# Performance work log

Measured on AMD Instinct MI355X. Metric: run time of the kernel, lower is better.

Reference implementation:

```python
import jax, jax.numpy as jnp
import numpy as np

EPS = 1e-08
SLOPE = 0.01  # LeakyReLU default negative_slope
B = 2097152
H = 32

def leaky_relu(x):
    return jnp.where(x >= 0, x, SLOPE * x)

def gram_schmidt(v, w):
    # v, w: [b,3]
    v_on = v / (jnp.linalg.norm(v, axis=-1, keepdims=True) + EPS)
    proj = jnp.sum(w * v_on, axis=-1, keepdims=True) * v_on
    w_orth = w - proj
    w_on = w_orth / (jnp.linalg.norm(w_orth, axis=-1, keepdims=True) + EPS)
    u_on = jnp.cross(v_on, w_on)
    R = jnp.stack((v_on, w_on, u_on), axis=-1)  # [b,3,3]
    v_local = jnp.einsum('bji,bj->bi', R, v)    # R^T @ v
    w_local = jnp.einsum('bji,bj->bi', R, w)
    return R, v_local, w_local

def setup_inputs() -> dict:
    key = jax.random.key(0)
    ks = jax.random.split(key, 12)
    std = 0.0001  # init_weights() normal std
    return {
        'v': jax.random.normal(ks[0], (B, 3), jnp.float32),
        'w': jax.random.normal(ks[1], (B, 3), jnp.float32),
        'W1': jax.random.normal(ks[2], (H, 3), jnp.float32) * std,
        'b1': jax.random.normal(ks[3], (H,), jnp.float32) * std,
        'W2': jax.random.normal(ks[4], (H, H), jnp.float32) * std,
        'b2': jax.random.normal(ks[5], (H,), jnp.float32) * std,
        'Wd1': jax.random.normal(ks[6], (H, H), jnp.float32) * std,
        'bd1': jax.random.normal(ks[7], (H,), jnp.float32) * std,
        'Wd2': jax.random.normal(ks[8], (3, H), jnp.float32) * std,
        'bd2': jax.random.normal(ks[9], (3,), jnp.float32) * std,
        'bias': jnp.array([[0.0, 0.0, -9.81]], jnp.float32),
    }

def reference(v, w, W1, b1, W2, b2, Wd1, bd1, Wd2, bd2, bias):
    shapes = v.shape
    b = shapes[0]
    v = v.reshape(b, 3)
    w = w.reshape(b, 3)
    R, v_local, w_local = gram_schmidt(v, w)
    feat = jnp.concatenate([v_local[..., :1], w_local[..., :2]], axis=-1)  # [b,3]
    h1 = leaky_relu(feat @ W1.T + b1)           # [b,H]
    h = leaky_relu(h1 @ W2.T + b2) * h1         # [b,H]
    y = leaky_relu(h @ Wd1.T + bd1) @ Wd2.T + bd2  # [b,3]
    y = jnp.einsum('bij,bj->bi', R, y) + bias
    return y.reshape(shapes)
```

## Files before the change

kernel.cpp:

```cpp
#include <hip/hip_runtime.h>

typedef __attribute__((ext_vector_type(8))) short short8;
typedef __attribute__((ext_vector_type(4))) float f32x4;
typedef __attribute__((ext_vector_type(2))) float f32x2;
typedef __attribute__((ext_vector_type(4))) unsigned int u32x4;

static __device__ __forceinline__ unsigned int fbits(float f) {
    union { float f; unsigned int u; } v; v.f = f; return v.u;
}
static __device__ __forceinline__ float bitsf(unsigned int u) {
    union { float f; unsigned int u; } v; v.u = u; return v.f;
}
static __device__ __forceinline__ unsigned int pkbf(float lo, float hi) {
    return __builtin_amdgcn_perm(fbits(hi), fbits(lo), 0x07060302u);
}
static __device__ __forceinline__ float leaky(float x) { return fmaxf(x, 0.01f * x); }
static __device__ __forceinline__ float rsqrt_nr(float x) {
    const float r = __builtin_amdgcn_rsqf(x);
    return r * (1.5f - (0.5f * x) * (r * r));
}
static __device__ __forceinline__ f32x2 pk_mul_v(f32x2 a, f32x2 b) {
    f32x2 d; asm("v_pk_mul_f32 %0, %1, %2" : "=v"(d) : "v"(a), "v"(b)); return d;
}
static __device__ __forceinline__ f32x2 pk_fma_v(f32x2 a, f32x2 b, f32x2 c) {
    f32x2 d; asm("v_pk_fma_f32 %0, %1, %2, %3" : "=v"(d) : "v"(a), "v"(b), "v"(c)); return d;
}


struct Rot { float a0,a1,a2,c0,c1,c2,u0,u1,u2; };

static __device__ __forceinline__ Rot gs_feat(
    const float* __restrict__ vin, const float* __restrict__ win,
    int row, unsigned int* __restrict__ dst)
{
    const float v0 = vin[3*row+0], v1 = vin[3*row+1], v2 = vin[3*row+2];
    const float w0 = win[3*row+0], w1 = win[3*row+1], w2 = win[3*row+2];
    const float sv  = v0*v0 + v1*v1 + v2*v2;
    const float rnv = rsqrt_nr(sv);
    const float a0 = v0*rnv, a1 = v1*rnv, a2 = v2*rnv;
    const float proj = w0*a0 + w1*a1 + w2*a2;
    const float o0 = w0 - proj*a0, o1 = w1 - proj*a1, o2 = w2 - proj*a2;
    const float sw  = o0*o0 + o1*o1 + o2*o2;
    const float rnw = rsqrt_nr(sw);
    const float c0 = o0*rnw, c1 = o1*rnw, c2 = o2*rnw;
    const float u0 = a1*c2 - a2*c1;
    const float u1 = a2*c0 - a0*c2;
    const float u2 = a0*c1 - a1*c0;
    *(u32x4*)(dst)     = (u32x4){ fbits(sv*rnv) >> 16, fbits(proj) >> 16,
                                  fbits(sw*rnw) >> 16, 0u };
    *(u32x4*)(dst + 4) = (u32x4){ 0u, 0u, 0u, 0u };
    return {a0,a1,a2,c0,c1,c2,u0,u1,u2};
}

#define TILE_CHAIN(LB, YS0, YS1, YS2)                                              \
    {                                                                              \
        float y0k = 0.f, y1k = 0.f, y2k = 0.f;                                     \
        _Pragma("unroll")                                                          \
        for (int t = 0; t < 4; ++t) {                                              \
            const u32x4 bfr = *(const u32x4*)(                                     \
                &featlds[((LB) + wbase + 16*t + i15) * 8 + ko]);                   \
            const short8 featfrag = __builtin_bit_cast(short8, bfr);               \
            const f32x4 z1lo = __builtin_amdgcn_mfma_f32_16x16x32_bf16(            \
                fW1lo, featfrag, cb1lo, 0, 0, 0);                                  \
            const f32x4 z1hi = __builtin_amdgcn_mfma_f32_16x16x32_bf16(            \
                fW1hi, featfrag, cb1hi, 0, 0, 0);                                  \
            const float h1l0 = leaky(z1lo[0]), h1l1 = leaky(z1lo[1]);              \
            const float h1l2 = leaky(z1lo[2]), h1l3 = leaky(z1lo[3]);              \
            const float h1h0 = leaky(z1hi[0]), h1h1 = leaky(z1hi[1]);              \
            const float h1h2 = leaky(z1hi[2]), h1h3 = leaky(z1hi[3]);              \
            const short8 h1frag = __builtin_bit_cast(short8, (u32x4){              \
                pkbf(h1l0, h1h0), pkbf(h1l1, h1h1),                                \
                pkbf(h1l2, h1h2), pkbf(h1l3, h1h3) });                             \
            const f32x4 z2lo = __builtin_amdgcn_mfma_f32_16x16x32_bf16(            \
                fW2lo, h1frag, cb2lo, 0, 0, 0);                                    \
            const f32x4 z2hi = __builtin_amdgcn_mfma_f32_16x16x32_bf16(            \
                fW2hi, h1frag, cb2hi, 0, 0, 0);                                    \
            const short8 h2frag = __builtin_bit_cast(short8, (u32x4){              \
                pkbf(leaky(z2lo[0]) * h1l0, leaky(z2hi[0]) * h1h0),                \
                pkbf(leaky(z2lo[1]) * h1l1, leaky(z2hi[1]) * h1h1),                \
                pkbf(leaky(z2lo[2]) * h1l2, leaky(z2hi[2]) * h1h2),                \
                pkbf(leaky(z2lo[3]) * h1l3, leaky(z2hi[3]) * h1h3) });             \
            const f32x4 z3lo = __builtin_amdgcn_mfma_f32_16x16x32_bf16(            \
                fWd1lo, h2frag, cbd1lo, 0, 0, 0);                                  \
            const f32x4 z3hi = __builtin_amdgcn_mfma_f32_16x16x32_bf16(            \
                fWd1hi, h2frag, cbd1hi, 0, 0, 0);                                  \
            f32x2 h30, h31, h32, h33;                                              \
            h30.x = leaky(z3lo[0]); h30.y = leaky(z3hi[0]);                        \
            h31.x = leaky(z3lo[1]); h31.y = leaky(z3hi[1]);                        \
            h32.x = leaky(z3lo[2]); h32.y = leaky(z3hi[2]);                        \
            h33.x = leaky(z3lo[3]); h33.y = leaky(z3hi[3]);                        \
            f32x2 P0 = pk_mul_v(w00, h30);                                         \
            f32x2 P1 = pk_mul_v(w10, h30);                                         \
            f32x2 P2 = pk_mul_v(w20, h30);                                         \
            P0 = pk_fma_v(w01, h31, P0); P1 = pk_fma_v(w11, h31, P1);              \
            P2 = pk_fma_v(w21, h31, P2);                                           \
            P0 = pk_fma_v(w02, h32, P0); P1 = pk_fma_v(w12, h32, P1);              \
            P2 = pk_fma_v(w22, h32, P2);                                           \
            P0 = pk_fma_v(w03, h33, P0); P1 = pk_fma_v(w13, h33, P1);              \
            P2 = pk_fma_v(w23, h33, P2);                                           \
            float s0 = P0.x + P0.y, s1 = P1.x + P1.y, s2 = P2.x + P2.y;            \
            s0 += __shfl_xor(s0, 16); s0 += __shfl_xor(s0, 32);                    \
            s1 += __shfl_xor(s1, 16); s1 += __shfl_xor(s1, 32);                    \
            s2 += __shfl_xor(s2, 16); s2 += __shfl_xor(s2, 32);                    \
            if (quad == t) { y0k = s0; y1k = s1; y2k = s2; }                       \
        }                                                                          \
        YS0 = y0k; YS1 = y1k; YS2 = y2k;                                           \
    }

__global__ __launch_bounds__(256, 3) void aero_mfma(
    const float* __restrict__ vin, const float* __restrict__ win,
    const float* __restrict__ gW1, const float* __restrict__ gb1,
    const float* __restrict__ gW2, const float* __restrict__ gb2,
    const float* __restrict__ gWd1, const float* __restrict__ gbd1,
    const float* __restrict__ gWd2, const float* __restrict__ gbd2,
    const float* __restrict__ gbias,
    float* __restrict__ out, int nrows)
{
    __shared__ unsigned int featlds[513 * 8];

    const int tid   = threadIdx.x;
    const int i15   = tid & 15;
    const int quad  = (tid >> 4) & 3;
    const int wbase = tid & 192;
    const int ko    = 4 * quad;

    const int base = blockIdx.x * 512;
    int rowA = base + tid;        if (rowA >= nrows) rowA = nrows - 1;
    int rowB = base + 256 + tid;  if (rowB >= nrows) rowB = nrows - 1;

    unsigned int a1lo[4] = {0,0,0,0}, a1hi[4] = {0,0,0,0};
    if (quad == 0) {
        #pragma unroll
        for (int j = 0; j < 3; ++j) {
            a1lo[j] = fbits(gW1[i15 * 3 + j]) >> 16;
            a1hi[j] = fbits(gW1[(16 + i15) * 3 + j]) >> 16;
        }
    }
    const short8 fW1lo = __builtin_bit_cast(short8, (u32x4){a1lo[0], a1lo[1], a1lo[2], a1lo[3]});
    const short8 fW1hi = __builtin_bit_cast(short8, (u32x4){a1hi[0], a1hi[1], a1hi[2], a1hi[3]});

    unsigned int a2lo[4], a2hi[4], a3lo[4], a3hi[4];
    {
        const float* p;
        p = gW2 + i15 * 32 + ko;
        { f32x4 xa = *(const f32x4*)p, xb = *(const f32x4*)(p + 16);
          #pragma unroll
          for (int j = 0; j < 4; ++j) a2lo[j] = pkbf(xa[j], xb[j]); }
        p = gW2 + (16 + i15) * 32 + ko;
        { f32x4 xa = *(const f32x4*)p, xb = *(const f32x4*)(p + 16);
          #pragma unroll
          for (int j = 0; j < 4; ++j) a2hi[j] = pkbf(xa[j], xb[j]); }
        p = gWd1 + i15 * 32 + ko;
        { f32x4 xa = *(const f32x4*)p, xb = *(const f32x4*)(p + 16);
          #pragma unroll
          for (int j = 0; j < 4; ++j) a3lo[j] = pkbf(xa[j], xb[j]); }
        p = gWd1 + (16 + i15) * 32 + ko;
        { f32x4 xa = *(const f32x4*)p, xb = *(const f32x4*)(p + 16);
          #pragma unroll
          for (int j = 0; j < 4; ++j) a3hi[j] = pkbf(xa[j], xb[j]); }
    }
    const short8 fW2lo  = __builtin_bit_cast(short8, (u32x4){a2lo[0], a2lo[1], a2lo[2], a2lo[3]});
    const short8 fW2hi  = __builtin_bit_cast(short8, (u32x4){a2hi[0], a2hi[1], a2hi[2], a2hi[3]});
    const short8 fWd1lo = __builtin_bit_cast(short8, (u32x4){a3lo[0], a3lo[1], a3lo[2], a3lo[3]});
    const short8 fWd1hi = __builtin_bit_cast(short8, (u32x4){a3hi[0], a3hi[1], a3hi[2], a3hi[3]});

    f32x2 w00, w01, w02, w03, w10, w11, w12, w13, w20, w21, w22, w23;
    {
        f32x4 xa, xb;
        xa = *(const f32x4*)(gWd2 + 0*32 + ko); xb = *(const f32x4*)(gWd2 + 0*32 + ko + 16);
        w00.x = xa[0]; w00.y = xb[0]; w01.x = xa[1]; w01.y = xb[1];
        w02.x = xa[2]; w02.y = xb[2]; w03.x = xa[3]; w03.y = xb[3];
        xa = *(const f32x4*)(gWd2 + 1*32 + ko); xb = *(const f32x4*)(gWd2 + 1*32 + ko + 16);
        w10.x = xa[0]; w10.y = xb[0]; w11.x = xa[1]; w11.y = xb[1];
        w12.x = xa[2]; w12.y = xb[2]; w13.x = xa[3]; w13.y = xb[3];
        xa = *(const f32x4*)(gWd2 + 2*32 + ko); xb = *(const f32x4*)(gWd2 + 2*32 + ko + 16);
        w20.x = xa[0]; w20.y = xb[0]; w21.x = xa[1]; w21.y = xb[1];
        w22.x = xa[2]; w22.y = xb[2]; w23.x = xa[3]; w23.y = xb[3];
    }
    const f32x4 cb1lo  = *(const f32x4*)(gb1  + ko);
    const f32x4 cb1hi  = *(const f32x4*)(gb1  + 16 + ko);
    const f32x4 cb2lo  = *(const f32x4*)(gb2  + ko);
    const f32x4 cb2hi  = *(const f32x4*)(gb2  + 16 + ko);
    const f32x4 cbd1lo = *(const f32x4*)(gbd1 + ko);
    const f32x4 cbd1hi = *(const f32x4*)(gbd1 + 16 + ko);

    const Rot RA = gs_feat(vin, win, rowA, &featlds[tid * 8]);
    const Rot RB = gs_feat(vin, win, rowB, &featlds[(256 + tid) * 8]);
    if (tid < 8) featlds[512 * 8 + tid] = 0u;
    __syncthreads();

    float yA0, yA1, yA2, yB0, yB1, yB2;
    TILE_CHAIN(0,   yA0, yA1, yA2);
    TILE_CHAIN(256, yB0, yB1, yB2);

    const float bd20 = gbd2[0], bd21 = gbd2[1], bd22 = gbd2[2];
    const float gbs0 = gbias[0], gbs1 = gbias[1], gbs2 = gbias[2];
    yA0 += bd20; yA1 += bd21; yA2 += bd22;
    yB0 += bd20; yB1 += bd21; yB2 += bd22;

    out[3*rowA + 0] = fmaf(RA.a0, yA0, fmaf(RA.c0, yA1, fmaf(RA.u0, yA2, gbs0)));
    out[3*rowA + 1] = fmaf(RA.a1, yA0, fmaf(RA.c1, yA1, fmaf(RA.u1, yA2, gbs1)));
    out[3*rowA + 2] = fmaf(RA.a2, yA0, fmaf(RA.c2, yA1, fmaf(RA.u2, yA2, gbs2)));
    out[3*rowB + 0] = fmaf(RB.a0, yB0, fmaf(RB.c0, yB1, fmaf(RB.u0, yB2, gbs0)));
    out[3*rowB + 1] = fmaf(RB.a1, yB0, fmaf(RB.c1, yB1, fmaf(RB.u1, yB2, gbs1)));
    out[3*rowB + 2] = fmaf(RB.a2, yB0, fmaf(RB.c2, yB1, fmaf(RB.u2, yB2, gbs2)));
}

extern "C" void kernel_launch(void* const* d_in, const int* in_sizes, int n_in,
                              void* d_out, int out_size, void* d_ws, size_t ws_size,
                              hipStream_t stream) {
    const float* v    = (const float*)d_in[0];
    const float* w    = (const float*)d_in[1];
    const float* W1   = (const float*)d_in[2];
    const float* b1   = (const float*)d_in[3];
    const float* W2   = (const float*)d_in[4];
    const float* b2   = (const float*)d_in[5];
    const float* Wd1  = (const float*)d_in[6];
    const float* bd1  = (const float*)d_in[7];
    const float* Wd2  = (const float*)d_in[8];
    const float* bd2  = (const float*)d_in[9];
    const float* bias = (const float*)d_in[10];

    const int nrows = in_sizes[0] / 3;
    dim3 block(256);
    dim3 grid((nrows + 511) / 512);
    hipLaunchKernelGGL(aero_mfma, grid, block, 0, stream,
                       v, w, W1, b1, W2, b2, Wd1, bd1, Wd2, bd2, bias,
                       (float*)d_out, nrows);
}
```

Before: 136.8 us.

## Compute final Wd2 layer with MFMA and interleave A/B tile chains

Replaces the packed-FP32 VALU dot products and butterfly shuffle reduction for the last 32->3 layer with a bf16 MFMA against a zero-padded Wd2 fragment, folding bd2 into the accumulator. The two row tiles A and B are now processed in one interleaved loop, so their independent MFMA chains can hide each other's latency. This removes the per-tile VALU work and cross-lane reductions, but adds bf16 rounding on the final hidden activations and Wd2 weights, and raises register pressure from keeping both chains live.

```diff
diff --git a/kernel.cpp b/kernel.cpp
--- a/kernel.cpp
+++ b/kernel.cpp
@@ -2,14 +2,10 @@
 
 typedef __attribute__((ext_vector_type(8))) short short8;
 typedef __attribute__((ext_vector_type(4))) float f32x4;
-typedef __attribute__((ext_vector_type(2))) float f32x2;
 typedef __attribute__((ext_vector_type(4))) unsigned int u32x4;
 
 static __device__ __forceinline__ unsigned int fbits(float f) {
     union { float f; unsigned int u; } v; v.f = f; return v.u;
-}
-static __device__ __forceinline__ float bitsf(unsigned int u) {
-    union { float f; unsigned int u; } v; v.u = u; return v.f;
 }
 static __device__ __forceinline__ unsigned int pkbf(float lo, float hi) {
     return __builtin_amdgcn_perm(fbits(hi), fbits(lo), 0x07060302u);
@@ -18,12 +14,6 @@
 static __device__ __forceinline__ float rsqrt_nr(float x) {
     const float r = __builtin_amdgcn_rsqf(x);
     return r * (1.5f - (0.5f * x) * (r * r));
-}
-static __device__ __forceinline__ f32x2 pk_mul_v(f32x2 a, f32x2 b) {
-    f32x2 d; asm("v_pk_mul_f32 %0, %1, %2" : "=v"(d) : "v"(a), "v"(b)); return d;
-}
-static __device__ __forceinline__ f32x2 pk_fma_v(f32x2 a, f32x2 b, f32x2 c) {
-    f32x2 d; asm("v_pk_fma_f32 %0, %1, %2, %3" : "=v"(d) : "v"(a), "v"(b), "v"(c)); return d;
 }
 
 
@@ -52,61 +42,6 @@
     return {a0,a1,a2,c0,c1,c2,u0,u1,u2};
 }
 
-#define TILE_CHAIN(LB, YS0, YS1, YS2)                                              \
-    {                                                                              \
-        float y0k = 0.f, y1k = 0.f, y2k = 0.f;                                     \
-        _Pragma("unroll")                                                          \
-        for (int t = 0; t < 4; ++t) {                                              \
-            const u32x4 bfr = *(const u32x4*)(                                     \
-                &featlds[((LB) + wbase + 16*t + i15) * 8 + ko]);                   \
-            const short8 featfrag = __builtin_bit_cast(short8, bfr);               \
-            const f32x4 z1lo = __builtin_amdgcn_mfma_f32_16x16x32_bf16(            \
-                fW1lo, featfrag, cb1lo, 0, 0, 0);                                  \
-            const f32x4 z1hi = __builtin_amdgcn_mfma_f32_16x16x32_bf16(            \
-                fW1hi, featfrag, cb1hi, 0, 0, 0);                                  \
-            const float h1l0 = leaky(z1lo[0]), h1l1 = leaky(z1lo[1]);              \
-            const float h1l2 = leaky(z1lo[2]), h1l3 = leaky(z1lo[3]);              \
-            const float h1h0 = leaky(z1hi[0]), h1h1 = leaky(z1hi[1]);              \
-            const float h1h2 = leaky(z1hi[2]), h1h3 = leaky(z1hi[3]);              \
-            const short8 h1frag = __builtin_bit_cast(short8, (u32x4){              \
-                pkbf(h1l0, h1h0), pkbf(h1l1, h1h1),                                \
-                pkbf(h1l2, h1h2), pkbf(h1l3, h1h3) });                             \
-            const f32x4 z2lo = __builtin_amdgcn_mfma_f32_16x16x32_bf16(            \
-                fW2lo, h1frag, cb2lo, 0, 0, 0);                                    \
-            const f32x4 z2hi = __builtin_amdgcn_mfma_f32_16x16x32_bf16(            \
-                fW2hi, h1frag, cb2hi, 0, 0, 0);                                    \
-            const short8 h2frag = __builtin_bit_cast(short8, (u32x4){              \
-                pkbf(leaky(z2lo[0]) * h1l0, leaky(z2hi[0]) * h1h0),                \
-                pkbf(leaky(z2lo[1]) * h1l1, leaky(z2hi[1]) * h1h1),                \
-                pkbf(leaky(z2lo[2]) * h1l2, leaky(z2hi[2]) * h1h2),                \
-                pkbf(leaky(z2lo[3]) * h1l3, leaky(z2hi[3]) * h1h3) });             \
-            const f32x4 z3lo = __builtin_amdgcn_mfma_f32_16x16x32_bf16(            \
-                fWd1lo, h2frag, cbd1lo, 0, 0, 0);                                  \
-            const f32x4 z3hi = __builtin_amdgcn_mfma_f32_16x16x32_bf16(            \
-                fWd1hi, h2frag, cbd1hi, 0, 0, 0);                                  \
-            f32x2 h30, h31, h32, h33;                                              \
-            h30.x = leaky(z3lo[0]); h30.y = leaky(z3hi[0]);                        \
-            h31.x = leaky(z3lo[1]); h31.y = leaky(z3hi[1]);                        \
-            h32.x = leaky(z3lo[2]); h32.y = leaky(z3hi[2]);                        \
-            h33.x = leaky(z3lo[3]); h33.y = leaky(z3hi[3]);                        \
-            f32x2 P0 = pk_mul_v(w00, h30);                                         \
-            f32x2 P1 = pk_mul_v(w10, h30);                                         \
-            f32x2 P2 = pk_mul_v(w20, h30);                                         \
-            P0 = pk_fma_v(w01, h31, P0); P1 = pk_fma_v(w11, h31, P1);              \
-            P2 = pk_fma_v(w21, h31, P2);                                           \
-            P0 = pk_fma_v(w02, h32, P0); P1 = pk_fma_v(w12, h32, P1);              \
-            P2 = pk_fma_v(w22, h32, P2);                                           \
-            P0 = pk_fma_v(w03, h33, P0); P1 = pk_fma_v(w13, h33, P1);              \
-            P2 = pk_fma_v(w23, h33, P2);                                           \
-            float s0 = P0.x + P0.y, s1 = P1.x + P1.y, s2 = P2.x + P2.y;            \
-            s0 += __shfl_xor(s0, 16); s0 += __shfl_xor(s0, 32);                    \
-            s1 += __shfl_xor(s1, 16); s1 += __shfl_xor(s1, 32);                    \
-            s2 += __shfl_xor(s2, 16); s2 += __shfl_xor(s2, 32);                    \
-            if (quad == t) { y0k = s0; y1k = s1; y2k = s2; }                       \
-        }                                                                          \
-        YS0 = y0k; YS1 = y1k; YS2 = y2k;                                           \
-    }
-
 __global__ __launch_bounds__(256, 3) void aero_mfma(
     const float* __restrict__ vin, const float* __restrict__ win,
     const float* __restrict__ gW1, const float* __restrict__ gb1,
@@ -164,40 +99,103 @@
     const short8 fWd1lo = __builtin_bit_cast(short8, (u32x4){a3lo[0], a3lo[1], a3lo[2], a3lo[3]});
     const short8 fWd1hi = __builtin_bit_cast(short8, (u32x4){a3hi[0], a3hi[1], a3hi[2], a3hi[3]});
 
-    f32x2 w00, w01, w02, w03, w10, w11, w12, w13, w20, w21, w22, w23;
-    {
-        f32x4 xa, xb;
-        xa = *(const f32x4*)(gWd2 + 0*32 + ko); xb = *(const f32x4*)(gWd2 + 0*32 + ko + 16);
-        w00.x = xa[0]; w00.y = xb[0]; w01.x = xa[1]; w01.y = xb[1];
-        w02.x = xa[2]; w02.y = xb[2]; w03.x = xa[3]; w03.y = xb[3];
-        xa = *(const f32x4*)(gWd2 + 1*32 + ko); xb = *(const f32x4*)(gWd2 + 1*32 + ko + 16);
-        w10.x = xa[0]; w10.y = xb[0]; w11.x = xa[1]; w11.y = xb[1];
-        w12.x = xa[2]; w12.y = xb[2]; w13.x = xa[3]; w13.y = xb[3];
-        xa = *(const f32x4*)(gWd2 + 2*32 + ko); xb = *(const f32x4*)(gWd2 + 2*32 + ko + 16);
-        w20.x = xa[0]; w20.y = xb[0]; w21.x = xa[1]; w21.y = xb[1];
-        w22.x = xa[2]; w22.y = xb[2]; w23.x = xa[3]; w23.y = xb[3];
-    }
+    unsigned int a4[4] = {0,0,0,0};
+    if (i15 < 3) {
+        const float* p4 = gWd2 + i15 * 32 + ko;
+        #pragma unroll
+        for (int j = 0; j < 4; ++j) a4[j] = pkbf(p4[j], p4[j + 16]);
+    }
+    const short8 fWd2 = __builtin_bit_cast(short8, (u32x4){a4[0], a4[1], a4[2], a4[3]});
+
     const f32x4 cb1lo  = *(const f32x4*)(gb1  + ko);
     const f32x4 cb1hi  = *(const f32x4*)(gb1  + 16 + ko);
     const f32x4 cb2lo  = *(const f32x4*)(gb2  + ko);
     const f32x4 cb2hi  = *(const f32x4*)(gb2  + 16 + ko);
     const f32x4 cbd1lo = *(const f32x4*)(gbd1 + ko);
     const f32x4 cbd1hi = *(const f32x4*)(gbd1 + 16 + ko);
+    f32x4 cbd2 = {0.f, 0.f, 0.f, 0.f};
+    if (quad == 0) { cbd2[0] = gbd2[0]; cbd2[1] = gbd2[1]; cbd2[2] = gbd2[2]; }
 
     const Rot RA = gs_feat(vin, win, rowA, &featlds[tid * 8]);
     const Rot RB = gs_feat(vin, win, rowB, &featlds[(256 + tid) * 8]);
     if (tid < 8) featlds[512 * 8 + tid] = 0u;
     __syncthreads();
 
-    float yA0, yA1, yA2, yB0, yB1, yB2;
-    TILE_CHAIN(0,   yA0, yA1, yA2);
-    TILE_CHAIN(256, yB0, yB1, yB2);
-
-    const float bd20 = gbd2[0], bd21 = gbd2[1], bd22 = gbd2[2];
+    float yA0 = 0.f, yA1 = 0.f, yA2 = 0.f, yB0 = 0.f, yB1 = 0.f, yB2 = 0.f;
+    #pragma unroll
+    for (int t = 0; t < 4; ++t) {
+        const int roff = (wbase + 16 * t + i15) * 8 + ko;
+        const u32x4 bfrA = *(const u32x4*)(&featlds[roff]);
+        const u32x4 bfrB = *(const u32x4*)(&featlds[256 * 8 + roff]);
+        const short8 ffA = __builtin_bit_cast(short8, bfrA);
+        const short8 ffB = __builtin_bit_cast(short8, bfrB);
+
+        const f32x4 z1loA = __builtin_amdgcn_mfma_f32_16x16x32_bf16(fW1lo, ffA, cb1lo, 0, 0, 0);
+        const f32x4 z1hiA = __builtin_amdgcn_mfma_f32_16x16x32_bf16(fW1hi, ffA, cb1hi, 0, 0, 0);
+        const f32x4 z1loB = __builtin_amdgcn_mfma_f32_16x16x32_bf16(fW1lo, ffB, cb1lo, 0, 0, 0);
+        const f32x4 z1hiB = __builtin_amdgcn_mfma_f32_16x16x32_bf16(fW1hi, ffB, cb1hi, 0, 0, 0);
+
+        const float h1l0A = leaky(z1loA[0]), h1l1A = leaky(z1loA[1]);
+        const float h1l2A = leaky(z1loA[2]), h1l3A = leaky(z1loA[3]);
+        const float h1h0A = leaky(z1hiA[0]), h1h1A = leaky(z1hiA[1]);
+        const float h1h2A = leaky(z1hiA[2]), h1h3A = leaky(z1hiA[3]);
+        const short8 h1fA = __builtin_bit_cast(short8, (u32x4){
+            pkbf(h1l0A, h1h0A), pkbf(h1l1A, h1h1A), pkbf(h1l2A, h1h2A), pkbf(h1l3A, h1h3A) });
+        const f32x4 z2loA = __builtin_amdgcn_mfma_f32_16x16x32_bf16(fW2lo, h1fA, cb2lo, 0, 0, 0);
+        const f32x4 z2hiA = __builtin_amdgcn_mfma_f32_16x16x32_bf16(fW2hi, h1fA, cb2hi, 0, 0, 0);
+
+        const float h1l0B = leaky(z1loB[0]), h1l1B = leaky(z1loB[1]);
+        const float h1l2B = leaky(z1loB[2]), h1l3B = leaky(z1loB[3]);
+        const float h1h0B = leaky(z1hiB[0]), h1h1B = leaky(z1hiB[1]);
+        const float h1h2B = leaky(z1hiB[2]), h1h3B = leaky(z1hiB[3]);
+        const short8 h1fB = __builtin_bit_cast(short8, (u32x4){
+            pkbf(h1l0B, h1h0B), pkbf(h1l1B, h1h1B), pkbf(h1l2B, h1h2B), pkbf(h1l3B, h1h3B) });
+        const f32x4 z2loB = __builtin_amdgcn_mfma_f32_16x16x32_bf16(fW2lo, h1fB, cb2lo, 0, 0, 0);
+        const f32x4 z2hiB = __builtin_amdgcn_mfma_f32_16x16x32_bf16(fW2hi, h1fB, cb2hi, 0, 0, 0);
+
+        const short8 h2fA = __builtin_bit_cast(short8, (u32x4){
+            pkbf(leaky(z2loA[0]) * h1l0A, leaky(z2hiA[0]) * h1h0A),
+            pkbf(leaky(z2loA[1]) * h1l1A, leaky(z2hiA[1]) * h1h1A),
+            pkbf(leaky(z2loA[2]) * h1l2A, leaky(z2hiA[2]) * h1h2A),
+            pkbf(leaky(z2loA[3]) * h1l3A, leaky(z2hiA[3]) * h1h3A) });
+        const f32x4 z3loA = __builtin_amdgcn_mfma_f32_16x16x32_bf16(fWd1lo, h2fA, cbd1lo, 0, 0, 0);
+        const f32x4 z3hiA = __builtin_amdgcn_mfma_f32_16x16x32_bf16(fWd1hi, h2fA, cbd1hi, 0, 0, 0);
+
+        const short8 h2fB = __builtin_bit_cast(short8, (u32x4){
+            pkbf(leaky(z2loB[0]) * h1l0B, leaky(z2hiB[0]) * h1h0B),
+            pkbf(leaky(z2loB[1]) * h1l1B, leaky(z2hiB[1]) * h1h1B),
+            pkbf(leaky(z2loB[2]) * h1l2B, leaky(z2hiB[2]) * h1h2B),
+            pkbf(leaky(z2loB[3]) * h1l3B, leaky(z2hiB[3]) * h1h3B) });
+        const f32x4 z3loB = __builtin_amdgcn_mfma_f32_16x16x32_bf16(fWd1lo, h2fB, cbd1lo, 0, 0, 0);
+        const f32x4 z3hiB = __builtin_amdgcn_mfma_f32_16x16x32_bf16(fWd1hi, h2fB, cbd1hi, 0, 0, 0);
+
+        const short8 h3fA = __builtin_bit_cast(short8, (u32x4){
+            pkbf(leaky(z3loA[0]), leaky(z3hiA[0])),
+            pkbf(leaky(z3loA[1]), leaky(z3hiA[1])),
+            pkbf(leaky(z3loA[2]), leaky(z3hiA[2])),
+            pkbf(leaky(z3loA[3]), leaky(z3hiA[3])) });
+        const f32x4 yAacc = __builtin_amdgcn_mfma_f32_16x16x32_bf16(fWd2, h3fA, cbd2, 0, 0, 0);
+
+        const short8 h3fB = __builtin_bit_cast(short8, (u32x4){
+            pkbf(leaky(z3loB[0]), leaky(z3hiB[0])),
+            pkbf(leaky(z3loB[1]), leaky(z3hiB[1])),
+            pkbf(leaky(z3loB[2]), leaky(z3hiB[2])),
+            pkbf(leaky(z3loB[3]), leaky(z3hiB[3])) });
+        const f32x4 yBacc = __builtin_amdgcn_mfma_f32_16x16x32_bf16(fWd2, h3fB, cbd2, 0, 0, 0);
+
+        const float sA0 = __shfl(yAacc[0], i15);
+        const float sA1 = __shfl(yAacc[1], i15);
+        const float sA2 = __shfl(yAacc[2], i15);
+        const float sB0 = __shfl(yBacc[0], i15);
+        const float sB1 = __shfl(yBacc[1], i15);
+        const float sB2 = __shfl(yBacc[2], i15);
+        if (quad == t) {
+            yA0 = sA0; yA1 = sA1; yA2 = sA2;
+            yB0 = sB0; yB1 = sB1; yB2 = sB2;
+        }
+    }
+
     const float gbs0 = gbias[0], gbs1 = gbias[1], gbs2 = gbias[2];
-    yA0 += bd20; yA1 += bd21; yA2 += bd22;
-    yB0 += bd20; yB1 += bd21; yB2 += bd22;
-
     out[3*rowA + 0] = fmaf(RA.a0, yA0, fmaf(RA.c0, yA1, fmaf(RA.u0, yA2, gbs0)));
     out[3*rowA + 1] = fmaf(RA.a1, yA0, fmaf(RA.c1, yA1, fmaf(RA.u1, yA2, gbs1)));
     out[3*rowA + 2] = fmaf(RA.a2, yA0, fmaf(RA.c2, yA1, fmaf(RA.u2, yA2, gbs2)));
```

New measurement: 133.7 us. 1.02x faster.
